# Kernel optimization log

Measured on AMD Instinct MI355X. Metric: run time of the kernel, lower is better.

Reference implementation:

```python
import jax, jax.numpy as jnp
import numpy as np

ALPHA = 10.0 / 100.0  # dt / tau

def setup_inputs() -> dict:
    key = jax.random.key(0)
    ks = jax.random.split(key, 5)
    seq_len, batch, input_size, hidden_size = 512, 64, 256, 1024
    x = jax.random.normal(ks[0], (seq_len, batch, input_size), dtype=jnp.float32)
    h0 = jnp.zeros((batch, hidden_size), dtype=jnp.float32)
    Wx = jax.random.normal(ks[1], (hidden_size, input_size), dtype=jnp.float32) / np.sqrt(input_size)
    bx = jax.random.normal(ks[2], (hidden_size,), dtype=jnp.float32) * 0.01
    Wh = jax.random.normal(ks[3], (hidden_size, hidden_size), dtype=jnp.float32) / np.sqrt(hidden_size)
    bh = jax.random.normal(ks[4], (hidden_size,), dtype=jnp.float32) * 0.01
    return {"x": x, "h0": h0, "Wx": Wx, "bx": bx, "Wh": Wh, "bh": bh}

def reference(x, h0, Wx, bx, Wh, bh):
    # Precompute input projection for all timesteps in one GEMM: [S,B,H]
    xproj = jnp.einsum('sbi,hi->sbh', x, Wx) + bx

    def step(h, xp_t):
        h_new = jax.nn.relu(xp_t + h @ Wh.T + bh)
        h = h * (1.0 - ALPHA) + h_new * ALPHA
        return h, h

    h_final, output = jax.lax.scan(step, h0, xproj)
    return output, h_final
```

## Files before the change

### kernel.cpp

```cpp
#include <hip/hip_runtime.h>
#include <stdint.h>

#define S_LEN 512
#define BATCH 64
#define INSZ  256
#define HID   1024
#define BH    (BATCH*HID)
#define NPIPE 8
#define ROWSP 8
#define NCG   32
#define SMEM_BYTES (131072 + 16384)
#define WS_PLANES_OFF 4096
#define PLANE_STRIDE (ROWSP*HID)
#define WS_NEEDED (WS_PLANES_OFF + NPIPE*2*2*PLANE_STRIDE*2)
#define FLAG_IDX(p, c) ((p)*128 + ((c)>>3)*32 + ((c)&7))

typedef __attribute__((ext_vector_type(8))) short short8;
typedef __attribute__((ext_vector_type(4))) short short4v;
typedef __attribute__((ext_vector_type(4))) float f32x4;
typedef __attribute__((ext_vector_type(4))) float f4;
typedef __attribute__((ext_vector_type(4))) unsigned int u32x4;

__device__ __forceinline__ uint32_t bf16_rne(float x) {
  uint32_t u = __float_as_uint(x);
  return (u + 0x7fffu + ((u >> 16) & 1u)) >> 16;
}
__device__ __forceinline__ void cvt_pair(float v, short& h, short& l) {
  uint32_t hb = bf16_rne(v);
  float hf = __uint_as_float(hb << 16);
  uint32_t lb = bf16_rne(v - hf);
  h = (short)hb; l = (short)lb;
}
__device__ __forceinline__ void cvt8(f4 a0, f4 a1, short8& hi, short8& lo) {
  #pragma unroll
  for (int e = 0; e < 4; ++e) { short h, l; cvt_pair(a0[e], h, l); hi[e] = h; lo[e] = l; }
  #pragma unroll
  for (int e = 0; e < 4; ++e) { short h, l; cvt_pair(a1[e], h, l); hi[4+e] = h; lo[4+e] = l; }
}

#define MFMA(A, B, C) __builtin_amdgcn_mfma_f32_16x16x32_bf16((A), (B), (C), 0, 0, 0)
#define WAIT_VM0() do { asm volatile("s_waitcnt vmcnt(0)" ::: "memory"); \
                        __builtin_amdgcn_sched_barrier(0); } while (0)

__device__ __forceinline__ void llc_load_f4(f4& d, const float* p) {
  asm volatile("global_load_dwordx4 %0, %1, off sc0 sc1" : "=v"(d) : "v"(p) : "memory");
}
__device__ __forceinline__ void llc_load_s8(short8& d, const uint16_t* p) {
  asm volatile("global_load_dwordx4 %0, %1, off sc0 sc1" : "=v"(d) : "v"(p) : "memory");
}
__device__ __forceinline__ void llc_store_f4(float* p, f4 v) {
  asm volatile("global_store_dwordx4 %0, %1, off sc0 sc1" :: "v"(p), "v"(v) : "memory");
}
__device__ __forceinline__ void llc_store_s4(uint16_t* p, short4v v) {
  asm volatile("global_store_dwordx2 %0, %1, off sc0 sc1" :: "v"(p), "v"(v) : "memory");
}
__device__ __forceinline__ void llc_store_u16(uint16_t* p, uint32_t v) {
  asm volatile("global_store_short %0, %1, off sc0 sc1" :: "v"(p), "v"(v) : "memory");
}
__device__ __forceinline__ void llc_store_u32(uint32_t* p, uint32_t v) {
  asm volatile("global_store_dword %0, %1, off sc0 sc1" :: "v"(p), "v"(v) : "memory");
}
__device__ __forceinline__ uint32_t poll_min8(const uint32_t* p) {
  u32x4 a, b;
  asm volatile("global_load_dwordx4 %0, %2, off sc0 sc1\n\t"
               "global_load_dwordx4 %1, %2, off offset:16 sc0 sc1\n\t"
               "s_waitcnt vmcnt(0)"
               : "=&v"(a), "=&v"(b) : "v"(p) : "memory");
  uint32_t m = a.x;
  m = a.y < m ? a.y : m;  m = a.z < m ? a.z : m;  m = a.w < m ? a.w : m;
  m = b.x < m ? b.x : m;  m = b.y < m ? b.y : m;  m = b.z < m ? b.z : m;
  m = b.w < m ? b.w : m;
  return m;
}

__global__ void ctrnn_init(uint32_t* ws) {
  const int i = threadIdx.x;
  ws[i] = 0; ws[i + 256] = 0; ws[i + 512] = 0; ws[i + 768] = 0;
}

template<bool SPLIT>
__global__ __launch_bounds__(256, 1)
void ctrnn_main(const float* __restrict__ x,  const float* __restrict__ h0,
                const float* __restrict__ Wx, const float* __restrict__ bx,
                const float* __restrict__ Wh, const float* __restrict__ bh,
                float* __restrict__ out, uint32_t* ws)
{
  extern __shared__ char smem_raw[];
  short* pHi = (short*)smem_raw;
  short* pLo = pHi + 32768;
  float* red = (float*)(smem_raw + 131072);

  const int tid  = threadIdx.x;
  const int wg   = blockIdx.x;
  const int lane = tid & 63;
  const int wave = tid >> 6;
  const int l15  = lane & 15;
  const int kg   = lane >> 4;

  for (int tt = 0; tt < 2; ++tt) {
    const int t = wg * 2 + tt;
    if (tt) __syncthreads();
    {
      const float* xt = x + (size_t)t * (BATCH * INSZ);
      #pragma unroll
      for (int it = 0; it < 16; ++it) {
        const int flat4 = (it * 256 + tid) * 4;
        const int b = flat4 >> 8;
        const int k = flat4 & 255;
        f4 v = *(const f4*)(xt + b * INSZ + k);
        short4v hv, lv;
        #pragma unroll
        for (int e = 0; e < 4; ++e) { short h, l; cvt_pair(v[e], h, l); hv[e] = h; lv[e] = l; }
        const int si = b * 256 + (k ^ ((b & 7) << 3));
        *(short4v*)(pHi + si) = hv;
        *(short4v*)(pLo + si) = lv;
      }
    }
    __syncthreads();
    for (int ntl = 0; ntl < 16; ++ntl) {
      const int nt = wave * 16 + ntl;
      const int nn = nt * 16 + l15;
      f32x4 acc0 = {0,0,0,0}, acc1 = {0,0,0,0}, acc2 = {0,0,0,0}, acc3 = {0,0,0,0};
      #pragma unroll
      for (int kt = 0; kt < 8; ++kt) {
        const int k = kt * 32 + kg * 8;
        const float* wp = Wx + (size_t)nn * INSZ + k;
        short8 bhi8, blo8;
        cvt8(*(const f4*)wp, *(const f4*)(wp + 4), bhi8, blo8);
        const int swz = (l15 & 7) << 3;
        short8 a0h = *(const short8*)(pHi + (     l15) * 256 + (k ^ swz));
        short8 a0l = *(const short8*)(pLo + (     l15) * 256 + (k ^ swz));
        short8 a1h = *(const short8*)(pHi + (16 + l15) * 256 + (k ^ swz));
        short8 a1l = *(const short8*)(pLo + (16 + l15) * 256 + (k ^ swz));
        short8 a2h = *(const short8*)(pHi + (32 + l15) * 256 + (k ^ swz));
        short8 a2l = *(const short8*)(pLo + (32 + l15) * 256 + (k ^ swz));
        short8 a3h = *(const short8*)(pHi + (48 + l15) * 256 + (k ^ swz));
        short8 a3l = *(const short8*)(pLo + (48 + l15) * 256 + (k ^ swz));
        acc0 = MFMA(a0h, bhi8, acc0);
        acc1 = MFMA(a1h, bhi8, acc1);
        acc2 = MFMA(a2h, bhi8, acc2);
        acc3 = MFMA(a3h, bhi8, acc3);
        acc0 = MFMA(a0l, bhi8, acc0);
        acc1 = MFMA(a1l, bhi8, acc1);
        acc2 = MFMA(a2l, bhi8, acc2);
        acc3 = MFMA(a3l, bhi8, acc3);
        acc0 = MFMA(a0h, blo8, acc0);
        acc1 = MFMA(a1h, blo8, acc1);
        acc2 = MFMA(a2h, blo8, acc2);
        acc3 = MFMA(a3h, blo8, acc3);
      }
      const float bxn = bx[nn];
      float* op = out + (size_t)t * BH;
      #pragma unroll
      for (int i = 0; i < 4; ++i) {
        const int b0 = kg * 4 + i;
        op[(size_t)(     b0) * HID + nn] = acc0[i] + bxn;
        op[(size_t)(16 + b0) * HID + nn] = acc1[i] + bxn;
        op[(size_t)(32 + b0) * HID + nn] = acc2[i] + bxn;
        op[(size_t)(48 + b0) * HID + nn] = acc3[i] + bxn;
      }
    }
  }

  __syncthreads();
  const int pipe = wg >> 5;
  const int cg   = wg & 31;
  const int rbase = pipe * ROWSP;
  #pragma unroll
  for (int it = 0; it < 32; ++it) {
    const int flat4 = (it * 256 + tid) * 4;
    const int r = flat4 >> 10;
    const int k = flat4 & 1023;
    f4 w = *(const f4*)(Wh + (size_t)(cg * 32 + r) * HID + k);
    short4v hv, lv;
    #pragma unroll
    for (int e = 0; e < 4; ++e) { short h, l; cvt_pair(w[e], h, l); hv[e] = h; lv[e] = l; }
    const int si = r * 1024 + (k ^ ((r & 7) << 3));
    *(short4v*)(pHi + si) = hv;
    *(short4v*)(pLo + si) = lv;
  }

  uint16_t* planes = (uint16_t*)((char*)ws + WS_PLANES_OFF);

  if (SPLIT) {
    const int r = tid >> 5, c = tid & 31;
    const float v = h0[(size_t)(rbase + r) * HID + cg * 32 + c];
    uint32_t hb = bf16_rne(v);
    const bool vb = ((c & 3) == 1) || ((c & 3) == 3);
    if (vb) hb &= ~1u;
    float hf = __uint_as_float(hb << 16);
    uint32_t lb = bf16_rne(v - hf);
    if (vb) lb &= ~1u;
    uint16_t* bH = planes + ((pipe * 2 + 1) * 2 + 0) * PLANE_STRIDE + r * HID + cg * 32 + c;
    llc_store_u16(bH, hb & 0xffffu);
    llc_store_u16(bH + PLANE_STRIDE, lb & 0xffffu);
  }

  const int er = lane >> 3, ejc = lane & 7;
  f4 hp = {0,0,0,0}, bhv = {0,0,0,0};
  if (wave == 0) {
    hp  = *(const f4*)(h0 + (size_t)(rbase + er) * HID + cg * 32 + ejc * 4);
    bhv = *(const f4*)(bh + cg * 32 + ejc * 4);
  }

  asm volatile("s_waitcnt vmcnt(0)" ::: "memory");
  __syncthreads();

  uint32_t* gbar = ws + 8;
  if (tid == 0) {
    __hip_atomic_fetch_add(gbar, 1u, __ATOMIC_RELEASE, __HIP_MEMORY_SCOPE_AGENT);
    int spins = 0;
    while (__hip_atomic_load(gbar, __ATOMIC_RELAXED, __HIP_MEMORY_SCOPE_AGENT) < 256u) {
      __builtin_amdgcn_s_sleep(8);
      if (++spins > (1 << 20)) break;
    }
  }
  __syncthreads();
  __builtin_amdgcn_fence(__ATOMIC_ACQUIRE, "agent");

  uint32_t* flags = ws;
  uint32_t* myflag = flags + FLAG_IDX(pipe, cg);
  const uint32_t* pollbase = flags + pipe * 128 + wave * 32;

  for (int t = 0; t < S_LEN; ++t) {
    float* op = out + (size_t)t * BH;
    const int buf_r = (t + 1) & 1, buf_w = t & 1;

    f4 xv = {0,0,0,0};
    if (wave == 0)
      xv = *(const f4*)(op + (size_t)(rbase + er) * HID + cg * 32 + ejc * 4);

    if (t > 0 && lane == 0) {
      int spins = 0;
      while (poll_min8(pollbase) < (uint32_t)t) {
        if (++spins > 64) __builtin_amdgcn_s_sleep(1);
        if (spins > (1 << 20)) break;
      }
    }

    short8 ah[8], al[8];
    #pragma unroll
    for (int kk = 0; kk < 8; ++kk) { ah[kk] = (short8)0; al[kk] = (short8)0; }

    if (SPLIT) {
      const uint16_t* pH = planes + ((pipe * 2 + buf_r) * 2 + 0) * PLANE_STRIDE
                           + l15 * HID + wave * 256 + kg * 8;
      const uint16_t* pL = pH + PLANE_STRIDE;
      const uint32_t vb0 = (uint32_t)(t & 1);
      const uint32_t vb1 = (uint32_t)((t >> 1) & 1);
      int attempts = 0;
      for (;;) {
        if (l15 < 8) {
          #pragma unroll
          for (int kk = 0; kk < 8; ++kk) {
            llc_load_s8(ah[kk], pH + kk * 32);
            llc_load_s8(al[kk], pL + kk * 32);
          }
        }
        WAIT_VM0();
        uint32_t bad = 0;
        if (l15 < 8) {
          #pragma unroll
          for (int kk = 0; kk < 8; ++kk) {
            bad |= ((uint32_t)ah[kk][1] ^ vb0) & 1u;
            bad |= ((uint32_t)ah[kk][3] ^ vb1) & 1u;
            bad |= ((uint32_t)ah[kk][5] ^ vb0) & 1u;
            bad |= ((uint32_t)ah[kk][7] ^ vb1) & 1u;
            bad |= ((uint32_t)al[kk][1] ^ vb0) & 1u;
            bad |= ((uint32_t)al[kk][3] ^ vb1) & 1u;
            bad |= ((uint32_t)al[kk][5] ^ vb0) & 1u;
            bad |= ((uint32_t)al[kk][7] ^ vb1) & 1u;
          }
        }
        if (__all(bad == 0)) break;
        if (++attempts > (1 << 16)) break;
        if ((attempts & 3) == 3) __builtin_amdgcn_s_sleep(1);
        asm volatile("" : "+v"(pH), "+v"(pL));
      }
    } else {
      f4 a[8][2];
      #pragma unroll
      for (int kk = 0; kk < 8; ++kk) { a[kk][0] = (f4){0,0,0,0}; a[kk][1] = (f4){0,0,0,0}; }
      if (l15 < 8) {
        const float* hrow = (t ? (op - BH) : h0)
                            + (size_t)(rbase + l15) * HID + wave * 256 + kg * 8;
        #pragma unroll
        for (int kk = 0; kk < 8; ++kk) {
          llc_load_f4(a[kk][0], hrow + kk * 32);
          llc_load_f4(a[kk][1], hrow + kk * 32 + 4);
        }
      }
      WAIT_VM0();
      #pragma unroll
      for (int kk = 0; kk < 8; ++kk) cvt8(a[kk][0], a[kk][1], ah[kk], al[kk]);
    }

    f32x4 acc0 = {0,0,0,0}, acc1 = {0,0,0,0};
    #pragma unroll
    for (int kk = 0; kk < 8; ++kk) {
      const int k = wave * 256 + kk * 32 + kg * 8;
      const int si = (k ^ ((l15 & 7) << 3));
      short8 b0h = *(const short8*)(pHi + l15 * 1024 + si);
      short8 b0l = *(const short8*)(pLo + l15 * 1024 + si);
      short8 b1h = *(const short8*)(pHi + (16 + l15) * 1024 + si);
      short8 b1l = *(const short8*)(pLo + (16 + l15) * 1024 + si);
      acc0 = MFMA(ah[kk], b0h, acc0);
      acc0 = MFMA(al[kk], b0h, acc0);
      acc0 = MFMA(ah[kk], b0l, acc0);
      acc1 = MFMA(ah[kk], b1h, acc1);
      acc1 = MFMA(al[kk], b1h, acc1);
      acc1 = MFMA(ah[kk], b1l, acc1);
    }

    float* rb = red + buf_w * 2048;
    *(f32x4*)(rb + wave * 512 + lane * 4) = acc0;
    *(f32x4*)(rb + wave * 512 + 256 + lane * 4) = acc1;
    __syncthreads();

    if (wave == 0) {
      f4 s;
      #pragma unroll
      for (int e = 0; e < 4; ++e) {
        const int tc = ejc * 4 + e;
        const int idx = (tc >> 4) * 256 + (((er >> 2) * 16 + (tc & 15)) * 4) + (er & 3);
        float a0 = rb[idx] + rb[512 + idx];
        float a1 = rb[1024 + idx] + rb[1536 + idx];
        s[e] = a0 + a1;
      }
      f4 hn;
      #pragma unroll
      for (int e = 0; e < 4; ++e) hn[e] = fmaxf(xv[e] + s[e] + bhv[e], 0.0f);
      #pragma unroll
      for (int e = 0; e < 4; ++e) hp[e] = 0.9f * hp[e] + 0.1f * hn[e];

      if (SPLIT) {
        const uint32_t wb0 = (uint32_t)((t + 1) & 1);
        const uint32_t wb1 = (uint32_t)(((t + 1) >> 1) & 1);
        short4v h4, l4;
        #pragma unroll
        for (int e = 0; e < 4; ++e) {
          float v = hp[e];
          uint32_t hb = bf16_rne(v);
          if (e == 1) hb = (hb & ~1u) | wb0;
          if (e == 3) hb = (hb & ~1u) | wb1;
          float hf = __uint_as_float(hb << 16);
          uint32_t lb = bf16_rne(v - hf);
          if (e == 1) lb = (lb & ~1u) | wb0;
          if (e == 3) lb = (lb & ~1u) | wb1;
          h4[e] = (short)hb; l4[e] = (short)lb;
        }
        uint16_t* bH = planes + ((pipe * 2 + buf_w) * 2 + 0) * PLANE_STRIDE
                       + er * HID + cg * 32 + ejc * 4;
        llc_store_s4(bH, h4);
        llc_store_s4(bH + PLANE_STRIDE, l4);
        if (lane == 0) llc_store_u32(myflag, (uint32_t)(t + 1));
        *(f4*)(op + (size_t)(rbase + er) * HID + cg * 32 + ejc * 4) = hp;
        if (t == S_LEN - 1)
          *(f4*)(out + (size_t)S_LEN * BH + (size_t)(rbase + er) * HID + cg * 32 + ejc * 4) = hp;
      } else {
        llc_store_f4(op + (size_t)(rbase + er) * HID + cg * 32 + ejc * 4, hp);
        asm volatile("s_waitcnt vmcnt(0)" ::: "memory");
        if (lane == 0) llc_store_u32(myflag, (uint32_t)(t + 1));
        if (t == S_LEN - 1)
          llc_store_f4(out + (size_t)S_LEN * BH + (size_t)(rbase + er) * HID + cg * 32 + ejc * 4, hp);
      }
    }
  }
}

extern "C" void kernel_launch(void* const* d_in, const int* in_sizes, int n_in,
                              void* d_out, int out_size, void* d_ws, size_t ws_size,
                              hipStream_t stream) {
  (void)in_sizes; (void)n_in; (void)out_size;
  const float* x  = (const float*)d_in[0];
  const float* h0 = (const float*)d_in[1];
  const float* Wx = (const float*)d_in[2];
  const float* bx = (const float*)d_in[3];
  const float* Wh = (const float*)d_in[4];
  const float* bh = (const float*)d_in[5];
  float* out = (float*)d_out;
  uint32_t* ws = (uint32_t*)d_ws;

  ctrnn_init<<<1, 256, 0, stream>>>(ws);
  if (ws_size >= (size_t)WS_NEEDED) {
    hipFuncSetAttribute((const void*)ctrnn_main<true>,
                        hipFuncAttributeMaxDynamicSharedMemorySize, SMEM_BYTES);
    ctrnn_main<true><<<256, 256, SMEM_BYTES, stream>>>(x, h0, Wx, bx, Wh, bh, out, ws);
  } else {
    hipFuncSetAttribute((const void*)ctrnn_main<false>,
                        hipFuncAttributeMaxDynamicSharedMemorySize, SMEM_BYTES);
    ctrnn_main<false><<<256, 256, SMEM_BYTES, stream>>>(x, h0, Wx, bx, Wh, bh, out, ws);
  }
}
```

Before: 2.296 ms.

## Spread recurrence epilogue across all waves and publish step flag early

The per-step epilogue (reduction of partial sums, ReLU and leaky update, bf16 hi/lo split, plane and output stores) now runs on all 256 threads with one element each, instead of wave 0 handling four elements per lane. This shortens the serial tail on the critical path of every timestep. In the split-plane path, the readiness flag is now stored right after the reduction barrier, before the new h planes are written. That relies on the parity bits embedded in the plane values for consumers to detect stale data, which makes the protocol more fragile. The non-split path adds a block barrier before the flag store.

Measured after the change: 2.011 ms. -12.4%, faster.

```diff
diff --git a/kernel.cpp b/kernel.cpp
--- a/kernel.cpp
+++ b/kernel.cpp
@@ -48,11 +48,8 @@
 __device__ __forceinline__ void llc_load_s8(short8& d, const uint16_t* p) {
   asm volatile("global_load_dwordx4 %0, %1, off sc0 sc1" : "=v"(d) : "v"(p) : "memory");
 }
-__device__ __forceinline__ void llc_store_f4(float* p, f4 v) {
-  asm volatile("global_store_dwordx4 %0, %1, off sc0 sc1" :: "v"(p), "v"(v) : "memory");
-}
-__device__ __forceinline__ void llc_store_s4(uint16_t* p, short4v v) {
-  asm volatile("global_store_dwordx2 %0, %1, off sc0 sc1" :: "v"(p), "v"(v) : "memory");
+__device__ __forceinline__ void llc_store_f1(float* p, float v) {
+  asm volatile("global_store_dword %0, %1, off sc0 sc1" :: "v"(p), "v"(v) : "memory");
 }
 __device__ __forceinline__ void llc_store_u16(uint16_t* p, uint32_t v) {
   asm volatile("global_store_short %0, %1, off sc0 sc1" :: "v"(p), "v"(v) : "memory");
@@ -182,26 +179,24 @@
 
   uint16_t* planes = (uint16_t*)((char*)ws + WS_PLANES_OFF);
 
+  const int er2 = tid >> 5, ec2 = tid & 31;
+  const int gcol = cg * 32 + ec2;
+
   if (SPLIT) {
-    const int r = tid >> 5, c = tid & 31;
-    const float v = h0[(size_t)(rbase + r) * HID + cg * 32 + c];
+    const float v = h0[(size_t)(rbase + er2) * HID + gcol];
     uint32_t hb = bf16_rne(v);
-    const bool vb = ((c & 3) == 1) || ((c & 3) == 3);
+    const bool vb = ((ec2 & 3) == 1) || ((ec2 & 3) == 3);
     if (vb) hb &= ~1u;
     float hf = __uint_as_float(hb << 16);
     uint32_t lb = bf16_rne(v - hf);
     if (vb) lb &= ~1u;
-    uint16_t* bH = planes + ((pipe * 2 + 1) * 2 + 0) * PLANE_STRIDE + r * HID + cg * 32 + c;
+    uint16_t* bH = planes + ((pipe * 2 + 1) * 2 + 0) * PLANE_STRIDE + er2 * HID + gcol;
     llc_store_u16(bH, hb & 0xffffu);
     llc_store_u16(bH + PLANE_STRIDE, lb & 0xffffu);
   }
 
-  const int er = lane >> 3, ejc = lane & 7;
-  f4 hp = {0,0,0,0}, bhv = {0,0,0,0};
-  if (wave == 0) {
-    hp  = *(const f4*)(h0 + (size_t)(rbase + er) * HID + cg * 32 + ejc * 4);
-    bhv = *(const f4*)(bh + cg * 32 + ejc * 4);
-  }
+  float hp  = h0[(size_t)(rbase + er2) * HID + gcol];
+  const float bhc = bh[gcol];
 
   asm volatile("s_waitcnt vmcnt(0)" ::: "memory");
   __syncthreads();
@@ -221,14 +216,13 @@
   uint32_t* flags = ws;
   uint32_t* myflag = flags + FLAG_IDX(pipe, cg);
   const uint32_t* pollbase = flags + pipe * 128 + wave * 32;
+  const int gidx = (ec2 >> 4) * 256 + (((er2 >> 2) * 16 + (ec2 & 15)) * 4) + (er2 & 3);
 
   for (int t = 0; t < S_LEN; ++t) {
     float* op = out + (size_t)t * BH;
     const int buf_r = (t + 1) & 1, buf_w = t & 1;
 
-    f4 xv = {0,0,0,0};
-    if (wave == 0)
-      xv = *(const f4*)(op + (size_t)(rbase + er) * HID + cg * 32 + ejc * 4);
+    const float xvs = op[(size_t)(rbase + er2) * HID + gcol];
 
     if (t > 0 && lane == 0) {
       int spins = 0;
@@ -317,52 +311,37 @@
     *(f32x4*)(rb + wave * 512 + 256 + lane * 4) = acc1;
     __syncthreads();
 
-    if (wave == 0) {
-      f4 s;
-      #pragma unroll
-      for (int e = 0; e < 4; ++e) {
-        const int tc = ejc * 4 + e;
-        const int idx = (tc >> 4) * 256 + (((er >> 2) * 16 + (tc & 15)) * 4) + (er & 3);
-        float a0 = rb[idx] + rb[512 + idx];
-        float a1 = rb[1024 + idx] + rb[1536 + idx];
-        s[e] = a0 + a1;
-      }
-      f4 hn;
-      #pragma unroll
-      for (int e = 0; e < 4; ++e) hn[e] = fmaxf(xv[e] + s[e] + bhv[e], 0.0f);
-      #pragma unroll
-      for (int e = 0; e < 4; ++e) hp[e] = 0.9f * hp[e] + 0.1f * hn[e];
+    if (SPLIT && tid == 0) llc_store_u32(myflag, (uint32_t)(t + 1));
+
+    {
+      const float s = rb[gidx] + rb[512 + gidx] + rb[1024 + gidx] + rb[1536 + gidx];
+      const float hn = fmaxf(xvs + s + bhc, 0.0f);
+      hp = 0.9f * hp + 0.1f * hn;
 
       if (SPLIT) {
         const uint32_t wb0 = (uint32_t)((t + 1) & 1);
         const uint32_t wb1 = (uint32_t)(((t + 1) >> 1) & 1);
-        short4v h4, l4;
-        #pragma unroll
-        for (int e = 0; e < 4; ++e) {
-          float v = hp[e];
-          uint32_t hb = bf16_rne(v);
-          if (e == 1) hb = (hb & ~1u) | wb0;
-          if (e == 3) hb = (hb & ~1u) | wb1;
-          float hf = __uint_as_float(hb << 16);
-          uint32_t lb = bf16_rne(v - hf);
-          if (e == 1) lb = (lb & ~1u) | wb0;
-          if (e == 3) lb = (lb & ~1u) | wb1;
-          h4[e] = (short)hb; l4[e] = (short)lb;
-        }
+        uint32_t hb = bf16_rne(hp);
+        if ((ec2 & 3) == 1) hb = (hb & ~1u) | wb0;
+        else if ((ec2 & 3) == 3) hb = (hb & ~1u) | wb1;
+        float hf = __uint_as_float(hb << 16);
+        uint32_t lb = bf16_rne(hp - hf);
+        if ((ec2 & 3) == 1) lb = (lb & ~1u) | wb0;
+        else if ((ec2 & 3) == 3) lb = (lb & ~1u) | wb1;
         uint16_t* bH = planes + ((pipe * 2 + buf_w) * 2 + 0) * PLANE_STRIDE
-                       + er * HID + cg * 32 + ejc * 4;
-        llc_store_s4(bH, h4);
-        llc_store_s4(bH + PLANE_STRIDE, l4);
-        if (lane == 0) llc_store_u32(myflag, (uint32_t)(t + 1));
-        *(f4*)(op + (size_t)(rbase + er) * HID + cg * 32 + ejc * 4) = hp;
+                       + er2 * HID + gcol;
+        llc_store_u16(bH, hb & 0xffffu);
+        llc_store_u16(bH + PLANE_STRIDE, lb & 0xffffu);
+        op[(size_t)(rbase + er2) * HID + gcol] = hp;
         if (t == S_LEN - 1)
-          *(f4*)(out + (size_t)S_LEN * BH + (size_t)(rbase + er) * HID + cg * 32 + ejc * 4) = hp;
+          out[(size_t)S_LEN * BH + (size_t)(rbase + er2) * HID + gcol] = hp;
       } else {
-        llc_store_f4(op + (size_t)(rbase + er) * HID + cg * 32 + ejc * 4, hp);
+        llc_store_f1(op + (size_t)(rbase + er2) * HID + gcol, hp);
         asm volatile("s_waitcnt vmcnt(0)" ::: "memory");
-        if (lane == 0) llc_store_u32(myflag, (uint32_t)(t + 1));
+        __syncthreads();
+        if (tid == 0) llc_store_u32(myflag, (uint32_t)(t + 1));
         if (t == S_LEN - 1)
-          llc_store_f4(out + (size_t)S_LEN * BH + (size_t)(rbase + er) * HID + cg * 32 + ejc * 4, hp);
+          llc_store_f1(out + (size_t)S_LEN * BH + (size_t)(rbase + er2) * HID + gcol, hp);
       }
     }
   }
```
